# Kernel optimization log

Hardware: AMD Instinct MI355X
Metric: run time of the kernel (lower is better)

Reference implementation:

```python
import jax, jax.numpy as jnp
import numpy as np

N_NODES = 50000
N_EDGES = 800000
D_IN = 64
H1 = 64
H2 = 64
N_CLASSES = 10
N_GRAPHS = 500


def setup_inputs() -> dict:
    key = jax.random.key(0)
    ks = jax.random.split(key, 9)
    x = jax.random.normal(ks[0], (N_NODES, D_IN), dtype=jnp.float32)
    edge_index = jax.random.randint(ks[1], (2, N_EDGES), 0, N_NODES, dtype=jnp.int64)
    batch = jnp.sort(jax.random.randint(ks[2], (N_NODES,), 0, N_GRAPHS, dtype=jnp.int64))
    # Linear params (Kaiming-uniform-ish scale)
    def lin(k, fin, fout):
        kw, kb = jax.random.split(k)
        s = 1.0 / np.sqrt(fin)
        W = jax.random.uniform(kw, (fin, fout), minval=-s, maxval=s, dtype=jnp.float32)
        b = jax.random.uniform(kb, (fout,), minval=-s, maxval=s, dtype=jnp.float32)
        return W, b
    W1, b1 = lin(ks[3], D_IN, H1)
    W2, b2 = lin(ks[4], H1, H2)
    W3, b3 = lin(ks[5], H2, N_CLASSES)
    return {"x": x, "edge_index": edge_index, "batch": batch,
            "W1": W1, "b1": b1, "W2": W2, "b2": b2, "W3": W3, "b3": b3}


def _gin_conv(h, src, dst, W, b, eps=0.0):
    # sum aggregation of neighbor messages: msg[i] = sum_{(j->i)} h[j]
    agg = jax.ops.segment_sum(h[src], dst, num_segments=N_NODES)
    return ((1.0 + eps) * h + agg) @ W + b


def reference(x, edge_index, batch, W1, b1, W2, b2, W3, b3):
    src, dst = edge_index[0], edge_index[1]
    h = jax.nn.relu(_gin_conv(x, src, dst, W1, b1))
    h = jax.nn.relu(_gin_conv(h, src, dst, W2, b2))
    # global mean pool over graphs
    sums = jax.ops.segment_sum(h, batch, num_segments=N_GRAPHS)
    cnt = jax.ops.segment_sum(jnp.ones((N_NODES,), dtype=h.dtype), batch, num_segments=N_GRAPHS)
    pooled = sums / jnp.maximum(cnt, 1.0)[:, None]
    return pooled @ W3 + b3
```

## Files before the change

kernel.cpp:

```cpp
#include <hip/hip_runtime.h>
#include <hip/hip_bf16.h>
#include <hip/hip_fp16.h>


#define N_FEAT 64
#define CHUNK 4096
#define CAP 6144

typedef _Float16 f16;
typedef _Float16 half8 __attribute__((ext_vector_type(8)));
typedef float float4v __attribute__((ext_vector_type(4)));

__device__ inline f16 cvt_f16(float v) { return (f16)v; }
__device__ inline f16 cvt_f16(f16 v) { return v; }

template <typename TIN>
__global__ void gemm_mfma(const TIN* __restrict__ X, const float* __restrict__ W,
                          f16* __restrict__ Z, int nrows) {
    __shared__ f16 sX[64][72];
    __shared__ f16 sWT[64][72];
    int t = threadIdx.x;
    int base = blockIdx.x * 64;
    for (int idx = t; idx < 4096; idx += 256) {
        int k = idx >> 6, n = idx & 63;
        sWT[n][k] = (f16)W[idx];
    }
    for (int idx = t; idx < 4096; idx += 256) {
        int r = idx >> 6, c = idx & 63;
        int row = base + r;
        sX[r][c] = (row < nrows) ? cvt_f16(X[(size_t)row * 64 + c]) : (f16)0.f;
    }
    __syncthreads();
    int wave = t >> 6;
    int lane = t & 63;
    int quad = lane >> 4;
    int m16 = lane & 15;
    half8 a0 = *(const half8*)&sX[wave * 16 + m16][quad * 8];
    half8 a1 = *(const half8*)&sX[wave * 16 + m16][32 + quad * 8];
    float4v acc[4];
#pragma unroll
    for (int C = 0; C < 4; ++C) {
        half8 b0 = *(const half8*)&sWT[C * 16 + m16][quad * 8];
        half8 b1 = *(const half8*)&sWT[C * 16 + m16][32 + quad * 8];
        float4v d = {0.f, 0.f, 0.f, 0.f};
        d = __builtin_amdgcn_mfma_f32_16x16x32_f16(a0, b0, d, 0, 0, 0);
        d = __builtin_amdgcn_mfma_f32_16x16x32_f16(a1, b1, d, 0, 0, 0);
        acc[C] = d;
    }
#pragma unroll
    for (int reg = 0; reg < 4; ++reg) {
        int row = base + wave * 16 + quad * 4 + reg;
        if (row < nrows) {
#pragma unroll
            for (int C = 0; C < 4; ++C)
                Z[(size_t)row * 64 + C * 16 + m16] = (f16)acc[C][reg];
        }
    }
}

__global__ void bucket_scatter(const int* __restrict__ src, const int* __restrict__ dst,
                               int* __restrict__ ccur, int* __restrict__ staging, int E) {
    __shared__ int epack[CHUNK];
    __shared__ int ebkt[CHUNK];
    __shared__ int hist[256];
    __shared__ int base[256];
    int t = threadIdx.x;
    int begin = blockIdx.x * CHUNK;
    int cnt = min(CHUNK, E - begin);
    hist[t] = 0;
    __syncthreads();
    for (int i = t; i < cnt; i += 256) {
        int d = dst[begin + i];
        int s = src[begin + i];
        epack[i] = (s & 0xFFFF) | ((d & 255) << 16);
        ebkt[i] = d >> 8;
        atomicAdd(&hist[d >> 8], 1);
    }
    __syncthreads();
    int h = hist[t];
    if (h > 0) base[t] = atomicAdd(&ccur[t], h);
    hist[t] = 0;
    __syncthreads();
    for (int i = t; i < cnt; i += 256) {
        int b = ebkt[i];
        int off = base[b] + atomicAdd(&hist[b], 1);
        if (off < CAP) staging[(size_t)b * CAP + off] = epack[i];
    }
}

__global__ void bucket_finalize(const int* __restrict__ staging, const int* __restrict__ ccur,
                                int2* __restrict__ rowse, int* __restrict__ col, int N) {
    __shared__ int edges[CAP];
    __shared__ int hist[256];
    __shared__ int scan[256];
    __shared__ int cur[256];
    int b = blockIdx.x, t = threadIdx.x;
    int cnt = min(ccur[b], CAP);
    int sbase = b * CAP;
    hist[t] = 0;
    __syncthreads();
    for (int i = t; i < cnt; i += 256) {
        int e = staging[(size_t)sbase + i];
        edges[i] = e;
        atomicAdd(&hist[(e >> 16) & 255], 1);
    }
    __syncthreads();
    int v = hist[t];
    scan[t] = v;
    __syncthreads();
    for (int off = 1; off < 256; off <<= 1) {
        int u = (t >= off) ? scan[t - off] : 0;
        __syncthreads();
        scan[t] += u;
        __syncthreads();
    }
    int excl = scan[t] - v;
    cur[t] = excl;
    int node = b * 256 + t;
    if (node < N) rowse[node] = make_int2(sbase + excl, sbase + excl + v);
    __syncthreads();
    for (int i = t; i < cnt; i += 256) {
        int e = edges[i];
        int pos = sbase + atomicAdd(&cur[(e >> 16) & 255], 1);
        col[pos] = e & 0xFFFF;
    }
}

__global__ void gather_relu(const f16* __restrict__ Z, const int2* __restrict__ rowse,
                            const int* __restrict__ col, const float* __restrict__ bias,
                            f16* __restrict__ H, int n) {
    int node = (int)((blockIdx.x * blockDim.x + threadIdx.x) >> 6);
    if (node >= n) return;
    int lane = threadIdx.x & 63;
    int g = lane >> 4, l = lane & 15;
    int2 se = rowse[node];
    int lo = se.x, hi = se.y;
    const float2* Z2 = reinterpret_cast<const float2*>(Z);
    float ax = 0.f, ay = 0.f, az = 0.f, aw = 0.f;
    int idx[8];
#pragma unroll
    for (int i = 0; i < 8; ++i) {
        int j = lo + g + i * 4;
        idx[i] = (j < hi) ? col[j] : -1;
    }
#pragma unroll
    for (int i = 0; i < 8; ++i) {
        if (idx[i] >= 0) {
            float2 r = Z2[(size_t)idx[i] * 16 + l];
            float2 f0 = __half22float2(*(__half2*)&r.x);
            float2 f1 = __half22float2(*(__half2*)&r.y);
            ax += f0.x; ay += f0.y; az += f1.x; aw += f1.y;
        }
    }
    for (int j = lo + 32 + g; j < hi; j += 4) {
        float2 r = Z2[(size_t)col[j] * 16 + l];
        float2 f0 = __half22float2(*(__half2*)&r.x);
        float2 f1 = __half22float2(*(__half2*)&r.y);
        ax += f0.x; ay += f0.y; az += f1.x; aw += f1.y;
    }
    ax += __shfl_xor(ax, 16); ay += __shfl_xor(ay, 16);
    az += __shfl_xor(az, 16); aw += __shfl_xor(aw, 16);
    ax += __shfl_xor(ax, 32); ay += __shfl_xor(ay, 32);
    az += __shfl_xor(az, 32); aw += __shfl_xor(aw, 32);
    if (g == 0) {
        float2 sr = Z2[(size_t)node * 16 + l];
        float2 fs0 = __half22float2(*(__half2*)&sr.x);
        float2 fs1 = __half22float2(*(__half2*)&sr.y);
        float4 b = reinterpret_cast<const float4*>(bias)[l];
        __half2 o0 = __floats2half2_rn(fmaxf(fs0.x + ax + b.x, 0.f),
                                       fmaxf(fs0.y + ay + b.y, 0.f));
        __half2 o1 = __floats2half2_rn(fmaxf(fs1.x + az + b.z, 0.f),
                                       fmaxf(fs1.y + aw + b.w, 0.f));
        float2 outv;
        *(__half2*)&outv.x = o0;
        *(__half2*)&outv.y = o1;
        reinterpret_cast<float2*>(H)[(size_t)node * 16 + l] = outv;
    }
}

__global__ void pool_head(const f16* __restrict__ H, const int* __restrict__ batch,
                          const float* __restrict__ W3, const float* __restrict__ b3,
                          float* __restrict__ out, int n, int ncls) {
    int gidx = blockIdx.x;
    __shared__ int bounds[2];
    __shared__ float sred[4 * 64];
    __shared__ float row[64];
    int t = threadIdx.x;
    int w = t >> 6;
    int lane = t & 63;
    int g = lane >> 4, l = lane & 15;
    if (t < 2) {
        int target = gidx + t;
        int lo = 0, hi = n;
        while (lo < hi) { int m = (lo + hi) >> 1; if (batch[m] < target) lo = m + 1; else hi = m; }
        bounds[t] = lo;
    }
    __syncthreads();
    int lo = bounds[0], hi = bounds[1];
    const float2* H2 = reinterpret_cast<const float2*>(H);
    float ax = 0.f, ay = 0.f, az = 0.f, aw = 0.f;
    for (int i = lo + (w * 4 + g); i < hi; i += 16) {
        float2 raw = H2[(size_t)i * 16 + l];
        float2 f0 = __half22float2(*(__half2*)&raw.x);
        float2 f1 = __half22float2(*(__half2*)&raw.y);
        ax += f0.x; ay += f0.y; az += f1.x; aw += f1.y;
    }
    ax += __shfl_xor(ax, 16); ay += __shfl_xor(ay, 16);
    az += __shfl_xor(az, 16); aw += __shfl_xor(aw, 16);
    ax += __shfl_xor(ax, 32); ay += __shfl_xor(ay, 32);
    az += __shfl_xor(az, 32); aw += __shfl_xor(aw, 32);
    if (g == 0) {
        sred[w * 64 + l * 4 + 0] = ax;
        sred[w * 64 + l * 4 + 1] = ay;
        sred[w * 64 + l * 4 + 2] = az;
        sred[w * 64 + l * 4 + 3] = aw;
    }
    __syncthreads();
    if (w == 0) {
        float s = sred[lane] + sred[64 + lane] + sred[128 + lane] + sred[192 + lane];
        row[lane] = s / fmaxf((float)(hi - lo), 1.0f);
    }
    __syncthreads();
    if (t < ncls) {
        float o = b3[t];
#pragma unroll
        for (int k = 0; k < 64; ++k) o += row[k] * W3[k * ncls + t];
        out[gidx * ncls + t] = o;
    }
}

extern "C" void kernel_launch(void* const* d_in, const int* in_sizes, int n_in,
                              void* d_out, int out_size, void* d_ws, size_t ws_size,
                              hipStream_t stream) {
    const float* x     = (const float*)d_in[0];
    const int*   ei    = (const int*)d_in[1];
    const int*   batch = (const int*)d_in[2];
    const float* W1    = (const float*)d_in[3];
    const float* b1    = (const float*)d_in[4];
    const float* W2    = (const float*)d_in[5];
    const float* b2    = (const float*)d_in[6];
    const float* W3    = (const float*)d_in[7];
    const float* b3    = (const float*)d_in[8];
    float* out = (float*)d_out;

    const int N = in_sizes[0] / N_FEAT;
    const int E = in_sizes[1] / 2;
    const int NCLS = 10;
    const int G = out_size / NCLS;
    const int* src = ei;
    const int* dst = ei + E;
    const int nb = (N + 255) / 256;

    int*  staging = (int*)d_ws;
    int2* rowse   = (int2*)(staging + (size_t)nb * CAP);
    int*  col     = (int*)(rowse + N);
    int*  ccur    = col + (size_t)nb * CAP;
    f16*  zbuf    = (f16*)(ccur + 256);
    f16*  hbuf    = zbuf + (size_t)N * 64;

    const int gemmGrid = (N + 63) / 64;
    const int gatherGrid = (N + 3) / 4;
    const int scatGrid = (E + CHUNK - 1) / CHUNK;

    hipMemsetAsync(ccur, 0, 256 * sizeof(int), stream);
    bucket_scatter<<<scatGrid, 256, 0, stream>>>(src, dst, ccur, staging, E);
    bucket_finalize<<<nb, 256, 0, stream>>>(staging, ccur, rowse, col, N);

    gemm_mfma<float><<<gemmGrid, 256, 0, stream>>>(x, W1, zbuf, N);
    gather_relu<<<gatherGrid, 256, 0, stream>>>(zbuf, rowse, col, b1, hbuf, N);

    gemm_mfma<f16><<<gemmGrid, 256, 0, stream>>>(hbuf, W2, zbuf, N);
    gather_relu<<<gatherGrid, 256, 0, stream>>>(zbuf, rowse, col, b2, hbuf, N);

    pool_head<<<G, 256, 0, stream>>>(hbuf, batch, W3, b3, out, N, NCLS);
}
```

Baseline: 190.3 us.

## Fuse scatter with first GEMM, split features into planes, compact CSR

Several changes land together. The edge bucket scatter and the first GEMM now run as one launch, with blocks chosen by index, so the two independent stages overlap. The global atomic cursor and its memset are replaced by per-chunk subbuckets plus a count matrix that finalize prefix-sums. Features are stored as two 32-wide planes so each gather block reads half-rows and gets smaller per-plane working sets. Row pointers are packed into one 32-bit word and column indices shrink to 16 bits. Risks: degree is capped at 127 and each subbucket holds only 64 edges, so skewed inputs could drop edges; planar gathers also read each column index twice.

```diff
diff --git a/kernel.cpp b/kernel.cpp
--- a/kernel.cpp
+++ b/kernel.cpp
@@ -5,6 +5,7 @@
 
 #define N_FEAT 64
 #define CHUNK 4096
+#define SUBCAP 64
 #define CAP 6144
 
 typedef _Float16 f16;
@@ -14,21 +15,27 @@
 __device__ inline f16 cvt_f16(float v) { return (f16)v; }
 __device__ inline f16 cvt_f16(f16 v) { return v; }
 
-template <typename TIN>
-__global__ void gemm_mfma(const TIN* __restrict__ X, const float* __restrict__ W,
-                          f16* __restrict__ Z, int nrows) {
-    __shared__ f16 sX[64][72];
-    __shared__ f16 sWT[64][72];
-    int t = threadIdx.x;
-    int base = blockIdx.x * 64;
+template <typename TIN, bool PLANAR_IN>
+__device__ void gemm_body(f16 (*sX)[72], f16 (*sWT)[72],
+                          const TIN* __restrict__ X, const float* __restrict__ W,
+                          f16* __restrict__ Z, int nrows, size_t nstride,
+                          int bid, int t) {
+    int base = bid * 64;
     for (int idx = t; idx < 4096; idx += 256) {
-        int k = idx >> 6, n = idx & 63;
-        sWT[n][k] = (f16)W[idx];
+        int k = idx >> 6, n_ = idx & 63;
+        sWT[n_][k] = (f16)W[idx];
     }
     for (int idx = t; idx < 4096; idx += 256) {
         int r = idx >> 6, c = idx & 63;
         int row = base + r;
-        sX[r][c] = (row < nrows) ? cvt_f16(X[(size_t)row * 64 + c]) : (f16)0.f;
+        f16 v = (f16)0.f;
+        if (row < nrows) {
+            if (PLANAR_IN)
+                v = cvt_f16(X[(size_t)(c >> 5) * nstride + (size_t)row * 32 + (c & 31)]);
+            else
+                v = cvt_f16(X[(size_t)row * 64 + c]);
+        }
+        sX[r][c] = v;
     }
     __syncthreads();
     int wave = t >> 6;
@@ -52,58 +59,105 @@
         int row = base + wave * 16 + quad * 4 + reg;
         if (row < nrows) {
 #pragma unroll
-            for (int C = 0; C < 4; ++C)
-                Z[(size_t)row * 64 + C * 16 + m16] = (f16)acc[C][reg];
-        }
-    }
-}
-
-__global__ void bucket_scatter(const int* __restrict__ src, const int* __restrict__ dst,
-                               int* __restrict__ ccur, int* __restrict__ staging, int E) {
-    __shared__ int epack[CHUNK];
-    __shared__ int ebkt[CHUNK];
-    __shared__ int hist[256];
-    __shared__ int base[256];
+            for (int C = 0; C < 4; ++C) {
+                int plane = C >> 1;
+                int ip = (C & 1) * 16 + m16;
+                Z[(size_t)plane * nstride + (size_t)row * 32 + ip] = (f16)acc[C][reg];
+            }
+        }
+    }
+}
+
+struct SmemScat {
+    int epack[CHUNK];
+    unsigned char ebkt[CHUNK];
+    int hist[256];
+    int cur[256];
+};
+struct SmemGemm {
+    f16 sX[64][72];
+    f16 sWT[64][72];
+};
+union SmemA { SmemScat s; SmemGemm g; };
+
+__global__ void scatter_or_gemm(const int* __restrict__ src, const int* __restrict__ dst,
+                                int* __restrict__ staging, int* __restrict__ cnts,
+                                int E, int NBLK,
+                                const float* __restrict__ X, const float* __restrict__ W,
+                                f16* __restrict__ Z, int nrows, size_t nstride,
+                                int scatBlocks) {
+    __shared__ SmemA sm;
     int t = threadIdx.x;
-    int begin = blockIdx.x * CHUNK;
-    int cnt = min(CHUNK, E - begin);
-    hist[t] = 0;
-    __syncthreads();
-    for (int i = t; i < cnt; i += 256) {
-        int d = dst[begin + i];
-        int s = src[begin + i];
-        epack[i] = (s & 0xFFFF) | ((d & 255) << 16);
-        ebkt[i] = d >> 8;
-        atomicAdd(&hist[d >> 8], 1);
-    }
-    __syncthreads();
-    int h = hist[t];
-    if (h > 0) base[t] = atomicAdd(&ccur[t], h);
-    hist[t] = 0;
-    __syncthreads();
-    for (int i = t; i < cnt; i += 256) {
-        int b = ebkt[i];
-        int off = base[b] + atomicAdd(&hist[b], 1);
-        if (off < CAP) staging[(size_t)b * CAP + off] = epack[i];
-    }
-}
-
-__global__ void bucket_finalize(const int* __restrict__ staging, const int* __restrict__ ccur,
-                                int2* __restrict__ rowse, int* __restrict__ col, int N) {
+    if ((int)blockIdx.x < scatBlocks) {
+        int blk = blockIdx.x;
+        int begin = blk * CHUNK;
+        int cnt = min(CHUNK, E - begin);
+        sm.s.hist[t] = 0;
+        __syncthreads();
+        for (int i = t; i < cnt; i += 256) {
+            int d = dst[begin + i];
+            int s = src[begin + i];
+            sm.s.epack[i] = (s & 0xFFFF) | ((d & 255) << 16);
+            sm.s.ebkt[i] = (unsigned char)(d >> 8);
+            atomicAdd(&sm.s.hist[d >> 8], 1);
+        }
+        __syncthreads();
+        cnts[t * NBLK + blk] = sm.s.hist[t];
+        sm.s.cur[t] = 0;
+        __syncthreads();
+        for (int i = t; i < cnt; i += 256) {
+            int b = sm.s.ebkt[i];
+            int off = atomicAdd(&sm.s.cur[b], 1);
+            if (off < SUBCAP)
+                staging[((size_t)b * NBLK + blk) * SUBCAP + off] = sm.s.epack[i];
+        }
+    } else {
+        gemm_body<float, false>(sm.g.sX, sm.g.sWT, X, W, Z, nrows, nstride,
+                                blockIdx.x - scatBlocks, t);
+    }
+}
+
+__global__ void gemm_mfma_planar(const f16* __restrict__ X, const float* __restrict__ W,
+                                 f16* __restrict__ Z, int nrows, size_t nstride) {
+    __shared__ SmemGemm sm;
+    gemm_body<f16, true>(sm.sX, sm.sWT, X, W, Z, nrows, nstride, blockIdx.x, threadIdx.x);
+}
+
+__global__ void bucket_finalize(const int* __restrict__ staging, const int* __restrict__ cnts,
+                                unsigned int* __restrict__ rowpk, unsigned short* __restrict__ col16,
+                                int N, int NBLK) {
     __shared__ int edges[CAP];
+    __shared__ int pre[256];
+    __shared__ int cntA[256];
     __shared__ int hist[256];
     __shared__ int scan[256];
     __shared__ int cur[256];
     int b = blockIdx.x, t = threadIdx.x;
-    int cnt = min(ccur[b], CAP);
-    int sbase = b * CAP;
+    int c0 = (t < NBLK) ? cnts[b * NBLK + t] : 0;
+    cntA[t] = c0;
+    scan[t] = c0;
+    __syncthreads();
+    for (int off = 1; off < 256; off <<= 1) {
+        int u = (t >= off) ? scan[t - off] : 0;
+        __syncthreads();
+        scan[t] += u;
+        __syncthreads();
+    }
+    pre[t] = scan[t] - c0;
+    int total = scan[255];
+    __syncthreads();
+    int wave = t >> 6, lane = t & 63;
+    for (int blk = wave; blk < NBLK; blk += 4) {
+        int cc = cntA[blk];
+        int base = pre[blk];
+        if (lane < cc && base + lane < CAP)
+            edges[base + lane] = staging[((size_t)b * NBLK + blk) * SUBCAP + lane];
+    }
     hist[t] = 0;
     __syncthreads();
-    for (int i = t; i < cnt; i += 256) {
-        int e = staging[(size_t)sbase + i];
-        edges[i] = e;
-        atomicAdd(&hist[(e >> 16) & 255], 1);
-    }
+    int cnt = min(total, CAP);
+    for (int i = t; i < cnt; i += 256)
+        atomicAdd(&hist[(edges[i] >> 16) & 255], 1);
     __syncthreads();
     int v = hist[t];
     scan[t] = v;
@@ -117,56 +171,65 @@
     int excl = scan[t] - v;
     cur[t] = excl;
     int node = b * 256 + t;
-    if (node < N) rowse[node] = make_int2(sbase + excl, sbase + excl + v);
+    if (node < N) {
+        unsigned int start = (unsigned int)(b * CAP + excl);
+        rowpk[node] = (start << 7) | (unsigned int)min(v, 127);
+    }
     __syncthreads();
     for (int i = t; i < cnt; i += 256) {
         int e = edges[i];
-        int pos = sbase + atomicAdd(&cur[(e >> 16) & 255], 1);
-        col[pos] = e & 0xFFFF;
-    }
-}
-
-__global__ void gather_relu(const f16* __restrict__ Z, const int2* __restrict__ rowse,
-                            const int* __restrict__ col, const float* __restrict__ bias,
-                            f16* __restrict__ H, int n) {
-    int node = (int)((blockIdx.x * blockDim.x + threadIdx.x) >> 6);
+        int pos = b * CAP + atomicAdd(&cur[(e >> 16) & 255], 1);
+        col16[pos] = (unsigned short)(e & 0xFFFF);
+    }
+}
+
+__global__ void gather_relu(const f16* __restrict__ Z, const unsigned int* __restrict__ rowpk,
+                            const unsigned short* __restrict__ col16, const float* __restrict__ bias,
+                            f16* __restrict__ H, int n, size_t nstride) {
+    int wave = threadIdx.x >> 6;
+    int node = (int)(blockIdx.x >> 1) * 4 + wave;
     if (node >= n) return;
+    int plane = blockIdx.x & 1;
     int lane = threadIdx.x & 63;
-    int g = lane >> 4, l = lane & 15;
-    int2 se = rowse[node];
-    int lo = se.x, hi = se.y;
-    const float2* Z2 = reinterpret_cast<const float2*>(Z);
+    int g = lane >> 3;
+    int l = lane & 7;
+    unsigned int pk = rowpk[node];
+    int lo = (int)(pk >> 7);
+    int deg = (int)(pk & 127);
+    const float2* Zp = reinterpret_cast<const float2*>(Z + (size_t)plane * nstride);
     float ax = 0.f, ay = 0.f, az = 0.f, aw = 0.f;
-    int idx[8];
-#pragma unroll
-    for (int i = 0; i < 8; ++i) {
-        int j = lo + g + i * 4;
-        idx[i] = (j < hi) ? col[j] : -1;
-    }
-#pragma unroll
-    for (int i = 0; i < 8; ++i) {
+    int idx[4];
+#pragma unroll
+    for (int i = 0; i < 4; ++i) {
+        int j = g + i * 8;
+        idx[i] = (j < deg) ? (int)col16[lo + j] : -1;
+    }
+#pragma unroll
+    for (int i = 0; i < 4; ++i) {
         if (idx[i] >= 0) {
-            float2 r = Z2[(size_t)idx[i] * 16 + l];
+            float2 r = Zp[(size_t)idx[i] * 8 + l];
             float2 f0 = __half22float2(*(__half2*)&r.x);
             float2 f1 = __half22float2(*(__half2*)&r.y);
             ax += f0.x; ay += f0.y; az += f1.x; aw += f1.y;
         }
     }
-    for (int j = lo + 32 + g; j < hi; j += 4) {
-        float2 r = Z2[(size_t)col[j] * 16 + l];
+    for (int j = 32 + g; j < deg; j += 8) {
+        float2 r = Zp[(size_t)col16[lo + j] * 8 + l];
         float2 f0 = __half22float2(*(__half2*)&r.x);
         float2 f1 = __half22float2(*(__half2*)&r.y);
         ax += f0.x; ay += f0.y; az += f1.x; aw += f1.y;
     }
+    ax += __shfl_xor(ax, 8);  ay += __shfl_xor(ay, 8);
+    az += __shfl_xor(az, 8);  aw += __shfl_xor(aw, 8);
     ax += __shfl_xor(ax, 16); ay += __shfl_xor(ay, 16);
     az += __shfl_xor(az, 16); aw += __shfl_xor(aw, 16);
     ax += __shfl_xor(ax, 32); ay += __shfl_xor(ay, 32);
     az += __shfl_xor(az, 32); aw += __shfl_xor(aw, 32);
     if (g == 0) {
-        float2 sr = Z2[(size_t)node * 16 + l];
+        float2 sr = Zp[(size_t)node * 8 + l];
         float2 fs0 = __half22float2(*(__half2*)&sr.x);
         float2 fs1 = __half22float2(*(__half2*)&sr.y);
-        float4 b = reinterpret_cast<const float4*>(bias)[l];
+        float4 b = reinterpret_cast<const float4*>(bias)[plane * 8 + l];
         __half2 o0 = __floats2half2_rn(fmaxf(fs0.x + ax + b.x, 0.f),
                                        fmaxf(fs0.y + ay + b.y, 0.f));
         __half2 o1 = __floats2half2_rn(fmaxf(fs1.x + az + b.z, 0.f),
@@ -174,13 +237,13 @@
         float2 outv;
         *(__half2*)&outv.x = o0;
         *(__half2*)&outv.y = o1;
-        reinterpret_cast<float2*>(H)[(size_t)node * 16 + l] = outv;
+        reinterpret_cast<float2*>(H + (size_t)plane * nstride)[(size_t)node * 8 + l] = outv;
     }
 }
 
 __global__ void pool_head(const f16* __restrict__ H, const int* __restrict__ batch,
                           const float* __restrict__ W3, const float* __restrict__ b3,
-                          float* __restrict__ out, int n, int ncls) {
+                          float* __restrict__ out, int n, int ncls, size_t nstride) {
     int gidx = blockIdx.x;
     __shared__ int bounds[2];
     __shared__ float sred[4 * 64];
@@ -189,6 +252,7 @@
     int w = t >> 6;
     int lane = t & 63;
     int g = lane >> 4, l = lane & 15;
+    int plane = l >> 3, fl = l & 7;
     if (t < 2) {
         int target = gidx + t;
         int lo = 0, hi = n;
@@ -197,10 +261,10 @@
     }
     __syncthreads();
     int lo = bounds[0], hi = bounds[1];
-    const float2* H2 = reinterpret_cast<const float2*>(H);
+    const float2* Hp = reinterpret_cast<const float2*>(H + (size_t)plane * nstride);
     float ax = 0.f, ay = 0.f, az = 0.f, aw = 0.f;
     for (int i = lo + (w * 4 + g); i < hi; i += 16) {
-        float2 raw = H2[(size_t)i * 16 + l];
+        float2 raw = Hp[(size_t)i * 8 + fl];
         float2 f0 = __half22float2(*(__half2*)&raw.x);
         float2 f1 = __half22float2(*(__half2*)&raw.y);
         ax += f0.x; ay += f0.y; az += f1.x; aw += f1.y;
@@ -210,10 +274,11 @@
     ax += __shfl_xor(ax, 32); ay += __shfl_xor(ay, 32);
     az += __shfl_xor(az, 32); aw += __shfl_xor(aw, 32);
     if (g == 0) {
-        sred[w * 64 + l * 4 + 0] = ax;
-        sred[w * 64 + l * 4 + 1] = ay;
-        sred[w * 64 + l * 4 + 2] = az;
-        sred[w * 64 + l * 4 + 3] = aw;
+        int ch = plane * 32 + fl * 4;
+        sred[w * 64 + ch + 0] = ax;
+        sred[w * 64 + ch + 1] = ay;
+        sred[w * 64 + ch + 2] = az;
+        sred[w * 64 + ch + 3] = aw;
     }
     __syncthreads();
     if (w == 0) {
@@ -250,27 +315,24 @@
     const int* src = ei;
     const int* dst = ei + E;
     const int nb = (N + 255) / 256;
-
-    int*  staging = (int*)d_ws;
-    int2* rowse   = (int2*)(staging + (size_t)nb * CAP);
-    int*  col     = (int*)(rowse + N);
-    int*  ccur    = col + (size_t)nb * CAP;
-    f16*  zbuf    = (f16*)(ccur + 256);
-    f16*  hbuf    = zbuf + (size_t)N * 64;
+    const int NBLK = (E + CHUNK - 1) / CHUNK;
+    const size_t nstride = (size_t)N * 32;
+
+    int*            staging = (int*)d_ws;
+    int*            cnts    = staging + (size_t)nb * NBLK * SUBCAP;
+    unsigned int*   rowpk   = (unsigned int*)(cnts + (size_t)nb * NBLK);
+    unsigned short* col16   = (unsigned short*)(rowpk + N);
+    f16*            zbuf    = (f16*)(col16 + (size_t)nb * CAP);
+    f16*            hbuf    = zbuf + (size_t)N * 64;
 
     const int gemmGrid = (N + 63) / 64;
-    const int gatherGrid = (N + 3) / 4;
-    const int scatGrid = (E + CHUNK - 1) / CHUNK;
-
-    hipMemsetAsync(ccur, 0, 256 * sizeof(int), stream);
-    bucket_scatter<<<scatGrid, 256, 0, stream>>>(src, dst, ccur, staging, E);
-    bucket_finalize<<<nb, 256, 0, stream>>>(staging, ccur, rowse, col, N);
-
-    gemm_mfma<float><<<gemmGrid, 256, 0, stream>>>(x, W1, zbuf, N);
-    gather_relu<<<gatherGrid, 256, 0, stream>>>(zbuf, rowse, col, b1, hbuf, N);
-
-    gemm_mfma<f16><<<gemmGrid, 256, 0, stream>>>(hbuf, W2, zbuf, N);
-    gather_relu<<<gatherGrid, 256, 0, stream>>>(zbuf, rowse, col, b2, hbuf, N);
-
-    pool_head<<<G, 256, 0, stream>>>(hbuf, batch, W3, b3, out, N, NCLS);
-}
+    const int gatherGrid = 2 * ((N + 3) / 4);
+
+    scatter_or_gemm<<<NBLK + gemmGrid, 256, 0, stream>>>(
+        src, dst, staging, cnts, E, NBLK, x, W1, zbuf, N, nstride, NBLK);
+    bucket_finalize<<<nb, 256, 0, stream>>>(staging, cnts, rowpk, col16, N, NBLK);
+    gather_relu<<<gatherGrid, 256, 0, stream>>>(zbuf, rowpk, col16, b1, hbuf, N, nstride);
+    gemm_mfma_planar<<<gemmGrid, 256, 0, stream>>>(hbuf, W2, zbuf, N, nstride);
+    gather_relu<<<gatherGrid, 256, 0, stream>>>(zbuf, rowpk, col16, b2, hbuf, N, nstride);
+    pool_head<<<G, 256, 0, stream>>>(hbuf, batch, W3, b3, out, N, NCLS, nstride);
+}
```

New measurement: 206.0 us. 8.3% more time.
